# Kernel tuning notes

Measured on AMD Instinct MI355X. Metric: run time of the kernel, lower is better.

## Reference

```python
import jax, jax.numpy as jnp
import numpy as np

HEADS = 16
DIM_HEAD = 64
DIM = 1024
EPS = 1e-5


def _layernorm(x, g, b):
    mu = jnp.mean(x, axis=-1, keepdims=True)
    var = jnp.var(x, axis=-1, keepdims=True)
    return (x - mu) * jax.lax.rsqrt(var + EPS) * g + b


def setup_inputs() -> dict:
    key = jax.random.key(0)
    ks = jax.random.split(key, 8)
    inner = HEADS * DIM_HEAD  # 1024
    x = jax.random.normal(ks[0], (2, 2048, DIM), dtype=jnp.float32)
    w_qkv = jax.random.normal(ks[1], (DIM, inner * 3), dtype=jnp.float32) * (DIM ** -0.5)
    w_out = jax.random.normal(ks[2], (inner, DIM), dtype=jnp.float32) * (inner ** -0.5)
    ln1_g = jnp.ones((DIM,), jnp.float32)
    ln1_b = jnp.zeros((DIM,), jnp.float32)
    ln2_g = jnp.ones((DIM,), jnp.float32)
    ln2_b = jnp.zeros((DIM,), jnp.float32)
    return {"x": x, "ln1_g": ln1_g, "ln1_b": ln1_b, "w_qkv": w_qkv,
            "w_out": w_out, "ln2_g": ln2_g, "ln2_b": ln2_b}


def reference(x, ln1_g, ln1_b, w_qkv, w_out, ln2_g, ln2_b):
    b, n, _ = x.shape
    scale = DIM_HEAD ** -0.5
    xn = _layernorm(x, ln1_g, ln1_b)
    qkv = xn @ w_qkv  # [b, n, 3*inner]
    q, k, v = jnp.split(qkv, 3, axis=-1)
    # b n (h d) -> b h n d
    resh = lambda t: t.reshape(b, n, HEADS, DIM_HEAD).transpose(0, 2, 1, 3)
    q, k, v = resh(q) * scale, resh(k), resh(v)
    sim = jnp.einsum('bhid,bhjd->bhij', q, k)
    causal = jnp.tril(jnp.ones((n, n), dtype=bool))
    # masked_fill(triu(1), 0) followed by relu == relu masked to lower triangle
    attn = jnp.where(causal, jax.nn.relu(sim), 0.0)
    out = jnp.einsum('bhij,bhjd->bhid', attn, v)
    out = out.transpose(0, 2, 1, 3).reshape(b, n, HEADS * DIM_HEAD)
    return _layernorm(out @ w_out, ln2_g, ln2_b)
```

## Files before the change

### kernel.cpp

```cpp
#include <hip/hip_runtime.h>
#include <cstdint>
#include <cstddef>


typedef __bf16 bf16_t;
typedef __bf16 bf16x8 __attribute__((ext_vector_type(8)));
typedef __bf16 bf16x4 __attribute__((ext_vector_type(4)));
typedef float  f32x4  __attribute__((ext_vector_type(4)));

#define DEV_INLINE __device__ __forceinline__

DEV_INLINE void async_copy16(void* lds, const void* g) {
  __builtin_amdgcn_global_load_lds(
      (__attribute__((address_space(1))) void*)(g),
      (__attribute__((address_space(3))) void*)(lds), 16, 0, 0);
}

__global__ __launch_bounds__(256) void prep_kernel(
    const float* __restrict__ x, const float* __restrict__ g1,
    const float* __restrict__ b1, bf16_t* __restrict__ xn,
    const float* __restrict__ w_qkv, bf16_t* __restrict__ wqkvT,
    const float* __restrict__ w_out, bf16_t* __restrict__ woutT) {
  const int bid = blockIdx.x;
  const int t = threadIdx.x;
  if (bid < 4096) {
    const int w = t >> 6, l = t & 63;
    const float* xr = x + (size_t)bid * 1024;
    float4 v = *(const float4*)(xr + t * 4);
    float s  = v.x + v.y + v.z + v.w;
    float s2 = v.x * v.x + v.y * v.y + v.z * v.z + v.w * v.w;
    #pragma unroll
    for (int off = 32; off >= 1; off >>= 1) {
      s  += __shfl_down(s, off);
      s2 += __shfl_down(s2, off);
    }
    __shared__ float red[8];
    if (l == 0) { red[w] = s; red[4 + w] = s2; }
    __syncthreads();
    s  = red[0] + red[1] + red[2] + red[3];
    s2 = red[4] + red[5] + red[6] + red[7];
    float mu  = s * (1.0f / 1024.0f);
    float var = s2 * (1.0f / 1024.0f) - mu * mu;
    float rs  = rsqrtf(var + 1e-5f);
    float4 gv = *(const float4*)(g1 + t * 4);
    float4 bv = *(const float4*)(b1 + t * 4);
    bf16x4 o;
    o[0] = (bf16_t)((v.x - mu) * rs * gv.x + bv.x);
    o[1] = (bf16_t)((v.y - mu) * rs * gv.y + bv.y);
    o[2] = (bf16_t)((v.z - mu) * rs * gv.z + bv.z);
    o[3] = (bf16_t)((v.w - mu) * rs * gv.w + bv.w);
    *(bf16x4*)(xn + (size_t)bid * 1024 + t * 4) = o;
  } else {
    const float* wsrc; bf16_t* wdst; int N, tile;
    if (bid < 4864) { wsrc = w_qkv; wdst = wqkvT; N = 3072; tile = bid - 4096; }
    else            { wsrc = w_out; wdst = woutT; N = 1024; tile = bid - 4864; }
    const int ntiles = N >> 6;
    const int n0 = (tile % ntiles) * 64, k0 = (tile / ntiles) * 64;
    __shared__ __align__(16) float tl[64][68];
    #pragma unroll
    for (int c = 0; c < 4; ++c) {
      int idx = c * 256 + t;
      int r = idx >> 4, c4 = (idx & 15) * 4;
      *(float4*)&tl[r][c4] = *(const float4*)(wsrc + (size_t)(k0 + r) * N + n0 + c4);
    }
    __syncthreads();
    #pragma unroll
    for (int c = 0; c < 2; ++c) {
      int idx = c * 256 + t;
      int nl = idx >> 3, kc = (idx & 7) * 8;
      bf16x8 o;
      #pragma unroll
      for (int ii = 0; ii < 8; ++ii) o[ii] = (bf16_t)tl[kc + ii][nl];
      *(bf16x8*)(wdst + (size_t)(n0 + nl) * 1024 + k0 + kc) = o;
    }
  }
}

__global__ __launch_bounds__(256) void ln2_kernel(
    const bf16_t* __restrict__ z0, const bf16_t* __restrict__ z1,
    const float* __restrict__ g, const float* __restrict__ bta,
    float* __restrict__ out) {
  const int row = blockIdx.x;
  const int t = threadIdx.x, w = t >> 6, l = t & 63;
  bf16x4 a0 = *(const bf16x4*)(z0 + (size_t)row * 1024 + t * 4);
  bf16x4 a1 = *(const bf16x4*)(z1 + (size_t)row * 1024 + t * 4);
  float4 v;
  v.x = (float)a0[0] + (float)a1[0];
  v.y = (float)a0[1] + (float)a1[1];
  v.z = (float)a0[2] + (float)a1[2];
  v.w = (float)a0[3] + (float)a1[3];
  float s  = v.x + v.y + v.z + v.w;
  float s2 = v.x * v.x + v.y * v.y + v.z * v.z + v.w * v.w;
  #pragma unroll
  for (int off = 32; off >= 1; off >>= 1) {
    s  += __shfl_down(s, off);
    s2 += __shfl_down(s2, off);
  }
  __shared__ float red[8];
  if (l == 0) { red[w] = s; red[4 + w] = s2; }
  __syncthreads();
  s  = red[0] + red[1] + red[2] + red[3];
  s2 = red[4] + red[5] + red[6] + red[7];
  float mu  = s * (1.0f / 1024.0f);
  float var = s2 * (1.0f / 1024.0f) - mu * mu;
  float rs  = rsqrtf(var + 1e-5f);
  float4 gv = *(const float4*)(g + t * 4);
  float4 bv = *(const float4*)(bta + t * 4);
  float4 o;
  o.x = (v.x - mu) * rs * gv.x + bv.x;
  o.y = (v.y - mu) * rs * gv.y + bv.y;
  o.z = (v.z - mu) * rs * gv.z + bv.z;
  o.w = (v.w - mu) * rs * gv.w + bv.w;
  *(float4*)(out + (size_t)row * 1024 + t * 4) = o;
}

template <int EPI, int KSPLIT>
__global__ __launch_bounds__(256, 3) void gemm128_kernel(
    const bf16_t* __restrict__ A, const bf16_t* __restrict__ Bt,
    void* __restrict__ C0, void* __restrict__ C1, void* __restrict__ C2) {
  __shared__ __align__(16) bf16_t As[128 * 64];
  __shared__ __align__(16) bf16_t Bs[128 * 64];
  const int t = threadIdx.x;
  const int w = t >> 6, l = t & 63, l15 = l & 15, quad = l >> 4;
  const int wy = w >> 1, wx = w & 1;
  const int m0 = blockIdx.y * 128, n0 = blockIdx.x * 128;
  const int kz = (KSPLIT > 1) ? blockIdx.z : 0;
  const int kt0 = kz * (16 / KSPLIT), kt1 = kt0 + (16 / KSPLIT);

  const int r_l = l >> 3;
  const int u_src = (l & 7) ^ r_l;
  const int rswz = l15 & 7;

  f32x4 acc[4][4];
  #pragma unroll
  for (int i = 0; i < 4; ++i)
    #pragma unroll
    for (int j = 0; j < 4; ++j) acc[i][j] = (f32x4)0.0f;

  for (int kt = kt0; kt < kt1; ++kt) {
    __syncthreads();
    #pragma unroll
    for (int c = 0; c < 4; ++c) {
      int idx = w * 4 + c;
      int row = idx * 8 + r_l;
      async_copy16(&As[idx * 512], A + (size_t)(m0 + row) * 1024 + kt * 64 + u_src * 8);
      async_copy16(&Bs[idx * 512], Bt + (size_t)(n0 + row) * 1024 + kt * 64 + u_src * 8);
    }
    __syncthreads();
    #pragma unroll
    for (int kk = 0; kk < 2; ++kk) {
      bf16x8 af[4], bfr[4];
      #pragma unroll
      for (int i = 0; i < 4; ++i)
        af[i] = *(const bf16x8*)&As[(wy * 64 + i * 16 + l15) * 64 + (((kk * 4 + quad) ^ rswz) * 8)];
      #pragma unroll
      for (int j = 0; j < 4; ++j)
        bfr[j] = *(const bf16x8*)&Bs[(wx * 64 + j * 16 + l15) * 64 + (((kk * 4 + quad) ^ rswz) * 8)];
      #pragma unroll
      for (int i = 0; i < 4; ++i)
        #pragma unroll
        for (int j = 0; j < 4; ++j)
          acc[i][j] = __builtin_amdgcn_mfma_f32_16x16x32_bf16(af[i], bfr[j], acc[i][j], 0, 0, 0);
    }
  }

  if (EPI == 0) {
    bf16_t* C = (bf16_t*)(kz == 0 ? C0 : C1);
    #pragma unroll
    for (int i = 0; i < 4; ++i)
      #pragma unroll
      for (int j = 0; j < 4; ++j)
        #pragma unroll
        for (int r = 0; r < 4; ++r) {
          int m = m0 + wy * 64 + i * 16 + quad * 4 + r;
          int n = n0 + wx * 64 + j * 16 + l15;
          C[(size_t)m * 1024 + n] = (bf16_t)acc[i][j][r];
        }
  } else {
    int nb = n0 + wx * 64;
    int which = nb >> 10;
    int head = (nb & 1023) >> 6;
    const int bq = m0 >> 11;
    const int mb = (m0 & 2047) + wy * 64;
    if (which == 2) {
      bf16_t* dst = (bf16_t*)C2 + ((size_t)(bq * 16 + head)) * 64 * 2048;
      #pragma unroll
      for (int i = 0; i < 4; ++i)
        #pragma unroll
        for (int j = 0; j < 4; ++j) {
          bf16x4 pk;
          #pragma unroll
          for (int r = 0; r < 4; ++r) pk[r] = (bf16_t)acc[i][j][r];
          int d = j * 16 + l15;
          int pos = mb + i * 16 + quad * 4;
          *(bf16x4*)(dst + (size_t)d * 2048 + pos) = pk;
        }
    } else {
      bf16_t* dst = which == 0 ? (bf16_t*)C0 : (bf16_t*)C1;
      float sc = which == 0 ? 0.125f : 1.0f;
      #pragma unroll
      for (int i = 0; i < 4; ++i)
        #pragma unroll
        for (int j = 0; j < 4; ++j)
          #pragma unroll
          for (int r = 0; r < 4; ++r) {
            int pos = mb + i * 16 + quad * 4 + r;
            int d = j * 16 + l15;
            dst[(((size_t)(bq * 16 + head)) * 2048 + pos) * 64 + d] =
                (bf16_t)(acc[i][j][r] * sc);
          }
    }
  }
}

__global__ __launch_bounds__(256, 4) void gemm_n64_kernel(
    const bf16_t* __restrict__ A, const bf16_t* __restrict__ Bt,
    bf16_t* __restrict__ C0, bf16_t* __restrict__ C1) {
  __shared__ __align__(16) bf16_t As[128 * 64];
  __shared__ __align__(16) bf16_t Bs[64 * 64];
  const int t = threadIdx.x;
  const int w = t >> 6, l = t & 63, l15 = l & 15, quad = l >> 4;
  const int wy = w >> 1, wx = w & 1;
  const int m0 = blockIdx.y * 128, n0 = blockIdx.x * 64;
  const int kz = blockIdx.z;
  const int kt0 = kz * 8, kt1 = kt0 + 8;

  const int r_l = l >> 3;
  const int u_src = (l & 7) ^ r_l;
  const int rswz = l15 & 7;

  f32x4 acc[4][2];
  #pragma unroll
  for (int i = 0; i < 4; ++i)
    #pragma unroll
    for (int j = 0; j < 2; ++j) acc[i][j] = (f32x4)0.0f;

  for (int kt = kt0; kt < kt1; ++kt) {
    __syncthreads();
    #pragma unroll
    for (int c = 0; c < 6; ++c) {
      int op = w * 6 + c;
      if (op < 16) {
        int row = op * 8 + r_l;
        async_copy16(&As[op * 512], A + (size_t)(m0 + row) * 1024 + kt * 64 + u_src * 8);
      } else {
        int bidx = op - 16;
        int row = bidx * 8 + r_l;
        async_copy16(&Bs[bidx * 512], Bt + (size_t)(n0 + row) * 1024 + kt * 64 + u_src * 8);
      }
    }
    __syncthreads();
    #pragma unroll
    for (int kk = 0; kk < 2; ++kk) {
      bf16x8 af[4], bfr[2];
      #pragma unroll
      for (int i = 0; i < 4; ++i)
        af[i] = *(const bf16x8*)&As[(wy * 64 + i * 16 + l15) * 64 + (((kk * 4 + quad) ^ rswz) * 8)];
      #pragma unroll
      for (int j = 0; j < 2; ++j)
        bfr[j] = *(const bf16x8*)&Bs[(wx * 32 + j * 16 + l15) * 64 + (((kk * 4 + quad) ^ rswz) * 8)];
      #pragma unroll
      for (int i = 0; i < 4; ++i)
        #pragma unroll
        for (int j = 0; j < 2; ++j)
          acc[i][j] = __builtin_amdgcn_mfma_f32_16x16x32_bf16(af[i], bfr[j], acc[i][j], 0, 0, 0);
    }
  }

  bf16_t* C = (kz == 0) ? C0 : C1;
  #pragma unroll
  for (int i = 0; i < 4; ++i)
    #pragma unroll
    for (int j = 0; j < 2; ++j)
      #pragma unroll
      for (int r = 0; r < 4; ++r) {
        int m = m0 + wy * 64 + i * 16 + quad * 4 + r;
        int n = n0 + wx * 32 + j * 16 + l15;
        C[(size_t)m * 1024 + n] = (bf16_t)acc[i][j][r];
      }
}

__global__ __launch_bounds__(512, 2) void attn_kernel(
    const bf16_t* __restrict__ q, const bf16_t* __restrict__ k,
    const bf16_t* __restrict__ vT, bf16_t* __restrict__ out) {
  __shared__ __align__(16) bf16_t Ks[2][2][64 * 64];
  __shared__ __align__(16) bf16_t Vts[2][2][64 * 64];
  __shared__ __align__(16) bf16_t Ss[2][2][64 * 72];

  const int h = blockIdx.x, j = blockIdx.y, b = blockIdx.z;
  const int t = threadIdx.x;
  const int w = t >> 6, l = t & 63, l15 = l & 15, quad = l >> 4;
  const int pairSel = w >> 2;
  const int wl = w & 3;
  const size_t bh = (size_t)(b * 16 + h);
  const int r0 = pairSel ? 30 - 2 * j : 2 * j;
  const int r1 = r0 + 1;
  const int niter = 16 - j;

  const int r_l = l >> 3;
  const int u_g = (l & 7) ^ r_l;
  const int rswz = l15 & 7;

  auto stage_pair = [&](int buf, int i2) {
    #pragma unroll
    for (int c = 0; c < 4; ++c) {
      int op = w * 4 + c;
      int tau = op >> 4;
      int rem = op & 15;
      int mK = rem >> 3;
      int idx = rem & 7;
      int kt = 2 * i2 + tau;
      int row = idx * 8 + r_l;
      if (mK == 0)
        async_copy16(&Ks[buf][tau][idx * 512],
                     k + (bh * 2048 + kt * 64 + row) * 64 + u_g * 8);
      else
        async_copy16(&Vts[buf][tau][idx * 512],
                     vT + (bh * 64 + row) * 2048 + kt * 64 + u_g * 8);
    }
  };

  auto load_lds = [&](const bf16_t* Kb, const bf16_t* Vb,
                      bf16x8 (&bk)[2][4], bf16x8 (&bv)[2][4]) {
    #pragma unroll
    for (int kk = 0; kk < 2; ++kk)
      #pragma unroll
      for (int tj = 0; tj < 4; ++tj) {
        int u = ((kk * 4 + quad) ^ rswz) * 8;
        bk[kk][tj] = *(const bf16x8*)&Kb[(tj * 16 + l15) * 64 + u];
        bv[kk][tj] = *(const bf16x8*)&Vb[(tj * 16 + l15) * 64 + u];
      }
  };

  bf16x8 qa[2][2];
  {
    #pragma unroll
    for (int kk = 0; kk < 2; ++kk) {
      qa[0][kk] = *(const bf16x8*)(q + (bh * 2048 + r0 * 64 + wl * 16 + l15) * 64 + kk * 32 + quad * 8);
      qa[1][kk] = *(const bf16x8*)(q + (bh * 2048 + r1 * 64 + wl * 16 + l15) * 64 + kk * 32 + quad * 8);
    }
  }

  f32x4 acc0[4], acc1[4];
  #pragma unroll
  for (int tj = 0; tj < 4; ++tj) { acc0[tj] = (f32x4)0.0f; acc1[tj] = (f32x4)0.0f; }

  auto sU = [&](f32x4 (&sacc)[4], bf16x8 (&qf)[2], bf16x8 (&bk)[2][4]) {
    #pragma unroll
    for (int tj = 0; tj < 4; ++tj) sacc[tj] = (f32x4)0.0f;
    #pragma unroll
    for (int kk = 0; kk < 2; ++kk)
      #pragma unroll
      for (int tj = 0; tj < 4; ++tj)
        sacc[tj] = __builtin_amdgcn_mfma_f32_16x16x32_bf16(bk[kk][tj], qf[kk], sacc[tj], 0, 0, 0);
  };
  auto wU = [&](f32x4 (&sacc)[4], bool dg, bf16_t* SsBuf) {
    #pragma unroll
    for (int tj = 0; tj < 4; ++tj) {
      bf16x4 pk;
      #pragma unroll
      for (int r = 0; r < 4; ++r) {
        float v = fmaxf(sacc[tj][r], 0.0f);
        if (dg && (tj * 16 + quad * 4 + r > wl * 16 + l15)) v = 0.0f;
        pk[r] = (bf16_t)v;
      }
      *(bf16x4*)&SsBuf[(wl * 16 + l15) * 72 + tj * 16 + quad * 4] = pk;
    }
  };
  auto pU = [&](f32x4 (&accr)[4], bf16x8 (&bv)[2][4], const bf16_t* SsBuf) {
    #pragma unroll
    for (int kk = 0; kk < 2; ++kk) {
      bf16x8 as_ = *(const bf16x8*)&SsBuf[(wl * 16 + l15) * 72 + kk * 32 + quad * 8];
      #pragma unroll
      for (int tj = 0; tj < 4; ++tj)
        accr[tj] = __builtin_amdgcn_mfma_f32_16x16x32_bf16(bv[kk][tj], as_, accr[tj], 0, 0, 0);
    }
  };

  bf16_t* SsA = &Ss[pairSel][0][0];
  bf16_t* SsB = &Ss[pairSel][1][0];

  stage_pair(0, 0);
  for (int i = 0; i < niter; ++i) {
    __syncthreads();
    if (i + 1 < niter) stage_pair((i + 1) & 1, i + 1);
    const int buf = i & 1;
    #pragma unroll
    for (int tau = 0; tau < 2; ++tau) {
      const int kt = 2 * i + tau;
      if (kt > r1) continue;
      bf16x8 bk[2][4], bv[2][4];
      load_lds(Ks[buf][tau], Vts[buf][tau], bk, bv);
      if (kt < r1) {
        f32x4 s0[4], s1[4];
        sU(s0, qa[0], bk);
        sU(s1, qa[1], bk);
        wU(s0, kt == r0, SsA);
        wU(s1, false, SsB);
        pU(acc0, bv, SsA);
        pU(acc1, bv, SsB);
      } else {
        f32x4 s1[4];
        sU(s1, qa[1], bk);
        wU(s1, true, SsB); pU(acc1, bv, SsB);
      }
    }
  }

  #pragma unroll
  for (int tj = 0; tj < 4; ++tj) {
    bf16x4 p0, p1;
    #pragma unroll
    for (int r = 0; r < 4; ++r) { p0[r] = (bf16_t)acc0[tj][r]; p1[r] = (bf16_t)acc1[tj][r]; }
    int posA = r0 * 64 + wl * 16 + l15;
    int posB = r1 * 64 + wl * 16 + l15;
    int col = h * 64 + tj * 16 + quad * 4;
    *(bf16x4*)(out + ((size_t)b * 2048 + posA) * 1024 + col) = p0;
    *(bf16x4*)(out + ((size_t)b * 2048 + posB) * 1024 + col) = p1;
  }
}

extern "C" void kernel_launch(void* const* d_in, const int* in_sizes, int n_in,
                              void* d_out, int out_size, void* d_ws, size_t ws_size,
                              hipStream_t stream) {
  (void)in_sizes; (void)n_in; (void)out_size; (void)ws_size;
  const float* x     = (const float*)d_in[0];
  const float* ln1_g = (const float*)d_in[1];
  const float* ln1_b = (const float*)d_in[2];
  const float* w_qkv = (const float*)d_in[3];
  const float* w_out = (const float*)d_in[4];
  const float* ln2_g = (const float*)d_in[5];
  const float* ln2_b = (const float*)d_in[6];
  float* out = (float*)d_out;

  char* ws = (char*)d_ws;
  bf16_t* xn     = (bf16_t*)(ws + 0);
  bf16_t* wqkvT  = (bf16_t*)(ws + 8388608);
  bf16_t* woutT  = (bf16_t*)(ws + 14680064);
  bf16_t* qb     = (bf16_t*)(ws + 16777216);
  bf16_t* kb     = (bf16_t*)(ws + 25165824);
  bf16_t* vTb    = (bf16_t*)(ws + 41943040);
  bf16_t* ao     = (bf16_t*)(ws + 50331648);
  bf16_t* zb0    = (bf16_t*)(ws + 58720256);
  bf16_t* zb1    = (bf16_t*)(ws + 67108864);

  prep_kernel<<<5120, 256, 0, stream>>>(x, ln1_g, ln1_b, xn, w_qkv, wqkvT, w_out, woutT);
  gemm128_kernel<1, 1><<<dim3(24, 32), 256, 0, stream>>>(xn, wqkvT, qb, kb, vTb);
  attn_kernel<<<dim3(16, 8, 2), 512, 0, stream>>>(qb, kb, vTb, ao);
  gemm_n64_kernel<<<dim3(16, 32, 2), 256, 0, stream>>>(ao, woutT, zb0, zb1);
  ln2_kernel<<<4096, 256, 0, stream>>>(zb0, zb1, ln2_g, ln2_b, out);
}
```

Baseline: 170.6 us.

## Rewrite QKV GEMM as 256x256 tile with double-buffered async LDS prefetch

Replaces the 128x128 single-buffered QKV projection GEMM with a 256x256-tile, 512-thread kernel. It double-buffers LDS and spreads the next k-tile's async global-to-LDS loads across four MFMA phases, raising wave priority around the MFMA bursts. The goal is to hide global load latency behind compute and to reuse each loaded tile more. The cost is fewer blocks (192 for 256 CUs, one per CU given 128KB of LDS), which may leave some CUs idle.

After: 185.3 us. 1.09x slower.

```diff
diff --git a/kernel.cpp b/kernel.cpp
--- a/kernel.cpp
+++ b/kernel.cpp
@@ -114,102 +114,116 @@
   *(float4*)(out + (size_t)row * 1024 + t * 4) = o;
 }
 
-template <int EPI, int KSPLIT>
-__global__ __launch_bounds__(256, 3) void gemm128_kernel(
+__global__ __launch_bounds__(512, 1) void gemm256_kernel(
     const bf16_t* __restrict__ A, const bf16_t* __restrict__ Bt,
     void* __restrict__ C0, void* __restrict__ C1, void* __restrict__ C2) {
-  __shared__ __align__(16) bf16_t As[128 * 64];
-  __shared__ __align__(16) bf16_t Bs[128 * 64];
+  __shared__ __align__(16) bf16_t As[2][256 * 64];
+  __shared__ __align__(16) bf16_t Bs[2][256 * 64];
   const int t = threadIdx.x;
   const int w = t >> 6, l = t & 63, l15 = l & 15, quad = l >> 4;
-  const int wy = w >> 1, wx = w & 1;
-  const int m0 = blockIdx.y * 128, n0 = blockIdx.x * 128;
-  const int kz = (KSPLIT > 1) ? blockIdx.z : 0;
-  const int kt0 = kz * (16 / KSPLIT), kt1 = kt0 + (16 / KSPLIT);
+  const int wy = w >> 2, wx = w & 3;
+  const int m0 = blockIdx.y * 256, n0 = blockIdx.x * 256;
 
   const int r_l = l >> 3;
   const int u_src = (l & 7) ^ r_l;
   const int rswz = l15 & 7;
 
-  f32x4 acc[4][4];
-  #pragma unroll
-  for (int i = 0; i < 4; ++i)
+  f32x4 acc[8][4];
+  #pragma unroll
+  for (int i = 0; i < 8; ++i)
     #pragma unroll
     for (int j = 0; j < 4; ++j) acc[i][j] = (f32x4)0.0f;
 
-  for (int kt = kt0; kt < kt1; ++kt) {
-    __syncthreads();
-    #pragma unroll
-    for (int c = 0; c < 4; ++c) {
-      int idx = w * 4 + c;
-      int row = idx * 8 + r_l;
-      async_copy16(&As[idx * 512], A + (size_t)(m0 + row) * 1024 + kt * 64 + u_src * 8);
-      async_copy16(&Bs[idx * 512], Bt + (size_t)(n0 + row) * 1024 + kt * 64 + u_src * 8);
-    }
-    __syncthreads();
-    #pragma unroll
-    for (int kk = 0; kk < 2; ++kk) {
-      bf16x8 af[4], bfr[4];
-      #pragma unroll
-      for (int i = 0; i < 4; ++i)
-        af[i] = *(const bf16x8*)&As[(wy * 64 + i * 16 + l15) * 64 + (((kk * 4 + quad) ^ rswz) * 8)];
+  auto stage_call = [&](int buf, int kt, int c) {
+    int g = w * 8 + c;
+    if (g < 32) {
+      int row = g * 8 + r_l;
+      async_copy16(&As[buf][g * 512],
+                   A + (size_t)(m0 + row) * 1024 + kt * 64 + u_src * 8);
+    } else {
+      int gb = g - 32;
+      int row = gb * 8 + r_l;
+      async_copy16(&Bs[buf][gb * 512],
+                   Bt + (size_t)(n0 + row) * 1024 + kt * 64 + u_src * 8);
+    }
+  };
+
+  #pragma unroll
+  for (int c = 0; c < 8; ++c) stage_call(0, 0, c);
+  asm volatile("s_waitcnt vmcnt(0)" ::: "memory");
+  __builtin_amdgcn_s_barrier();
+
+  for (int kt = 0; kt < 16; ++kt) {
+    const int buf = kt & 1;
+    const bool more = (kt + 1 < 16);
+    bf16x8 bfr[4];
+    #pragma unroll
+    for (int ph = 0; ph < 4; ++ph) {
+      const int kk = ph >> 1, ihalf = ph & 1;
+      const int u = ((kk * 4 + quad) ^ rswz) * 8;
+      bf16x8 af[4];
+      if (ihalf == 0) {
+        #pragma unroll
+        for (int j = 0; j < 4; ++j)
+          bfr[j] = *(const bf16x8*)&Bs[buf][(wx * 64 + j * 16 + l15) * 64 + u];
+        #pragma unroll
+        for (int i2 = 0; i2 < 4; ++i2)
+          af[i2] = *(const bf16x8*)&As[buf][(wy * 128 + i2 * 16 + l15) * 64 + u];
+      } else {
+        #pragma unroll
+        for (int i2 = 0; i2 < 4; ++i2)
+          af[i2] = *(const bf16x8*)&As[buf][(wy * 128 + (4 + i2) * 16 + l15) * 64 + u];
+      }
+      if (more) {
+        stage_call(buf ^ 1, kt + 1, ph * 2);
+        stage_call(buf ^ 1, kt + 1, ph * 2 + 1);
+      }
+      __builtin_amdgcn_s_barrier();
+      __builtin_amdgcn_s_setprio(1);
+      #pragma unroll
+      for (int i2 = 0; i2 < 4; ++i2)
+        #pragma unroll
+        for (int j = 0; j < 4; ++j)
+          acc[ihalf * 4 + i2][j] =
+              __builtin_amdgcn_mfma_f32_16x16x32_bf16(af[i2], bfr[j], acc[ihalf * 4 + i2][j], 0, 0, 0);
+      __builtin_amdgcn_s_setprio(0);
+    }
+    if (more) asm volatile("s_waitcnt vmcnt(0)" ::: "memory");
+    __builtin_amdgcn_s_barrier();
+  }
+
+  int nb = n0 + wx * 64;
+  int which = nb >> 10;
+  int head = (nb & 1023) >> 6;
+  const int bq = m0 >> 11;
+  const int mb = (m0 & 2047) + wy * 128;
+  if (which == 2) {
+    bf16_t* dst = (bf16_t*)C2 + ((size_t)(bq * 16 + head)) * 64 * 2048;
+    #pragma unroll
+    for (int i = 0; i < 8; ++i)
+      #pragma unroll
+      for (int j = 0; j < 4; ++j) {
+        bf16x4 pk;
+        #pragma unroll
+        for (int r = 0; r < 4; ++r) pk[r] = (bf16_t)acc[i][j][r];
+        int d = j * 16 + l15;
+        int pos = mb + i * 16 + quad * 4;
+        *(bf16x4*)(dst + (size_t)d * 2048 + pos) = pk;
+      }
+  } else {
+    bf16_t* dst = which == 0 ? (bf16_t*)C0 : (bf16_t*)C1;
+    float sc = which == 0 ? 0.125f : 1.0f;
+    #pragma unroll
+    for (int i = 0; i < 8; ++i)
       #pragma unroll
       for (int j = 0; j < 4; ++j)
-        bfr[j] = *(const bf16x8*)&Bs[(wx * 64 + j * 16 + l15) * 64 + (((kk * 4 + quad) ^ rswz) * 8)];
-      #pragma unroll
-      for (int i = 0; i < 4; ++i)
-        #pragma unroll
-        for (int j = 0; j < 4; ++j)
-          acc[i][j] = __builtin_amdgcn_mfma_f32_16x16x32_bf16(af[i], bfr[j], acc[i][j], 0, 0, 0);
-    }
-  }
-
-  if (EPI == 0) {
-    bf16_t* C = (bf16_t*)(kz == 0 ? C0 : C1);
-    #pragma unroll
-    for (int i = 0; i < 4; ++i)
-      #pragma unroll
-      for (int j = 0; j < 4; ++j)
         #pragma unroll
         for (int r = 0; r < 4; ++r) {
-          int m = m0 + wy * 64 + i * 16 + quad * 4 + r;
-          int n = n0 + wx * 64 + j * 16 + l15;
-          C[(size_t)m * 1024 + n] = (bf16_t)acc[i][j][r];
+          int pos = mb + i * 16 + quad * 4 + r;
+          int d = j * 16 + l15;
+          dst[(((size_t)(bq * 16 + head)) * 2048 + pos) * 64 + d] =
+              (bf16_t)(acc[i][j][r] * sc);
         }
-  } else {
-    int nb = n0 + wx * 64;
-    int which = nb >> 10;
-    int head = (nb & 1023) >> 6;
-    const int bq = m0 >> 11;
-    const int mb = (m0 & 2047) + wy * 64;
-    if (which == 2) {
-      bf16_t* dst = (bf16_t*)C2 + ((size_t)(bq * 16 + head)) * 64 * 2048;
-      #pragma unroll
-      for (int i = 0; i < 4; ++i)
-        #pragma unroll
-        for (int j = 0; j < 4; ++j) {
-          bf16x4 pk;
-          #pragma unroll
-          for (int r = 0; r < 4; ++r) pk[r] = (bf16_t)acc[i][j][r];
-          int d = j * 16 + l15;
-          int pos = mb + i * 16 + quad * 4;
-          *(bf16x4*)(dst + (size_t)d * 2048 + pos) = pk;
-        }
-    } else {
-      bf16_t* dst = which == 0 ? (bf16_t*)C0 : (bf16_t*)C1;
-      float sc = which == 0 ? 0.125f : 1.0f;
-      #pragma unroll
-      for (int i = 0; i < 4; ++i)
-        #pragma unroll
-        for (int j = 0; j < 4; ++j)
-          #pragma unroll
-          for (int r = 0; r < 4; ++r) {
-            int pos = mb + i * 16 + quad * 4 + r;
-            int d = j * 16 + l15;
-            dst[(((size_t)(bq * 16 + head)) * 2048 + pos) * 64 + d] =
-                (bf16_t)(acc[i][j][r] * sc);
-          }
-    }
   }
 }
 
@@ -445,7 +459,7 @@
   bf16_t* zb1    = (bf16_t*)(ws + 67108864);
 
   prep_kernel<<<5120, 256, 0, stream>>>(x, ln1_g, ln1_b, xn, w_qkv, wqkvT, w_out, woutT);
-  gemm128_kernel<1, 1><<<dim3(24, 32), 256, 0, stream>>>(xn, wqkvT, qb, kb, vTb);
+  gemm256_kernel<<<dim3(12, 16), 512, 0, stream>>>(xn, wqkvT, qb, kb, vTb);
   attn_kernel<<<dim3(16, 8, 2), 512, 0, stream>>>(qb, kb, vTb, ao);
   gemm_n64_kernel<<<dim3(16, 32, 2), 256, 0, stream>>>(ao, woutT, zb0, zb1);
   ln2_kernel<<<4096, 256, 0, stream>>>(zb0, zb1, ln2_g, ln2_b, out);
```
